# Optimization experiments

Measured on AMD Instinct MI355X. Metric: run time of the kernel, lower is better.

The kernel has to match this reference:

```python
import jax, jax.numpy as jnp
import numpy as np

N_CLASSES = 80
SEG_LEN = 512          # boxes per class (uniform segments)
H = 128                # hidden_size
DH = 2 * H             # decoder hidden (= concat of bidirectional encoder final hiddens)
EMB = 32               # decoder_input_dim
SOS, EOS = 2, 3


def _gru_cell(x, h, Wih, Whh, bih, bhh):
    # PyTorch GRU cell math. x:(in,), h:(hid,), Wih:(3*hid,in), Whh:(3*hid,hid)
    gi = Wih @ x + bih
    gh = Whh @ h + bhh
    i_r, i_z, i_n = jnp.split(gi, 3)
    h_r, h_z, h_n = jnp.split(gh, 3)
    r = jax.nn.sigmoid(i_r + h_r)
    z = jax.nn.sigmoid(i_z + h_z)
    n = jnp.tanh(i_n + r * h_n)
    return (1.0 - z) * n + z * h


def _gru_seq(xs, h0, Wih, Whh, bih, bhh):
    # xs: (T, in); returns final hidden (hid,) and all hiddens (T, hid)
    def step(h, x):
        h2 = _gru_cell(x, h, Wih, Whh, bih, bhh)
        return h2, h2
    hT, hs = jax.lax.scan(step, h0, xs)
    return hT, hs

# vmap over the 80 classes (per-class weights)
_run_gru = jax.vmap(_gru_seq, in_axes=(0, 0, 0, 0, 0, 0))


def setup_inputs() -> dict:
    key = jax.random.key(0)
    ks = jax.random.split(key, 32)
    N = N_CLASSES * SEG_LEN
    s = 0.05
    inp = {
        "feat": jax.random.normal(ks[0], (N, 1024), jnp.float32),
        "score": jax.random.uniform(ks[1], (N, 1), jnp.float32),
        "box": jax.random.uniform(ks[2], (N, 4), jnp.float32),
        "origin_score": jax.random.uniform(ks[3], (N, 91), jnp.float32),
        "labels": jax.random.randint(ks[4], (N,), 0, 2, jnp.int64),
        "weights": jax.random.uniform(ks[5], (N,), jnp.float32),
        "unique_class": jnp.ones((N_CLASSES,), jnp.int64),
        "unique_class_len": jnp.arange(N_CLASSES + 1, dtype=jnp.int64) * SEG_LEN,
        # shared linears
        "appear_W": jax.random.normal(ks[6], (H, 1024), jnp.float32) * s,
        "appear_b": jnp.zeros((H,), jnp.float32),
        "featlin_W": jax.random.normal(ks[7], (H, H + 96), jnp.float32) * s,
        "featlin_b": jnp.zeros((H,), jnp.float32),
        # per-class bidirectional encoder GRUs
        "enc_Wih_f": jax.random.normal(ks[8], (N_CLASSES, 3 * H, H), jnp.float32) * s,
        "enc_Whh_f": jax.random.normal(ks[9], (N_CLASSES, 3 * H, H), jnp.float32) * s,
        "enc_bih_f": jnp.zeros((N_CLASSES, 3 * H), jnp.float32),
        "enc_bhh_f": jnp.zeros((N_CLASSES, 3 * H), jnp.float32),
        "enc_Wih_b": jax.random.normal(ks[10], (N_CLASSES, 3 * H, H), jnp.float32) * s,
        "enc_Whh_b": jax.random.normal(ks[11], (N_CLASSES, 3 * H, H), jnp.float32) * s,
        "enc_bih_b": jnp.zeros((N_CLASSES, 3 * H), jnp.float32),
        "enc_bhh_b": jnp.zeros((N_CLASSES, 3 * H), jnp.float32),
        # decoder
        "dec_emb": jax.random.normal(ks[12], (4, EMB), jnp.float32) * s,
        "dec_Wih": jax.random.normal(ks[13], (N_CLASSES, 3 * DH, EMB), jnp.float32) * s,
        "dec_Whh": jax.random.normal(ks[14], (N_CLASSES, 3 * DH, DH), jnp.float32) * s,
        "dec_bih": jnp.zeros((N_CLASSES, 3 * DH), jnp.float32),
        "dec_bhh": jnp.zeros((N_CLASSES, 3 * DH), jnp.float32),
        "out_W": jax.random.normal(ks[15], (4, DH), jnp.float32) * s,
        "out_b": jnp.zeros((4,), jnp.float32),
    }
    return inp


def reference(feat, score, box, origin_score, labels, weights, unique_class,
              unique_class_len, appear_W, appear_b, featlin_W, featlin_b,
              enc_Wih_f, enc_Whh_f, enc_bih_f, enc_bhh_f,
              enc_Wih_b, enc_Whh_b, enc_bih_b, enc_bhh_b,
              dec_emb, dec_Wih, dec_Whh, dec_bih, dec_bhh, out_W, out_b):
    # --- shared feature encoding ---
    x = jax.nn.relu(feat @ appear_W.T + appear_b)                    # (N, H)
    allf = jnp.concatenate([x, score, box, origin_score], axis=1)    # (N, H+96)
    enc_feat = jax.nn.relu(allf @ featlin_W.T + featlin_b)           # (N, H)

    # --- per-class bidirectional encoder (uniform segments) ---
    seg = enc_feat.reshape(N_CLASSES, SEG_LEN, H)
    eos = jnp.ones((N_CLASSES, 1, H), enc_feat.dtype)                # encoder_EOS = ones
    enc_in = jnp.concatenate([seg, eos], axis=1)                     # (80, L+1, H)
    h0 = jnp.zeros((N_CLASSES, H), enc_feat.dtype)
    h_f, _ = _run_gru(enc_in, h0, enc_Wih_f, enc_Whh_f, enc_bih_f, enc_bhh_f)
    h_b, _ = _run_gru(enc_in[:, ::-1], h0, enc_Wih_b, enc_Whh_b, enc_bih_b, enc_bhh_b)
    dec_h0 = jnp.concatenate([h_f, h_b], axis=-1)                    # (80, 2H)

    # --- per-class decoder with teacher forcing (SOS then gold labels) ---
    emb = dec_emb[labels].reshape(N_CLASSES, SEG_LEN, EMB)
    sos = jnp.broadcast_to(dec_emb[SOS], (N_CLASSES, 1, EMB))
    dec_in = jnp.concatenate([sos, emb], axis=1)                     # (80, L+1, EMB)
    _, dec_hs = _run_gru(dec_in, dec_h0, dec_Wih, dec_Whh, dec_bih, dec_bhh)

    logits = dec_hs.reshape(-1, DH) @ out_W.T + out_b                # (80*(L+1), 4)
    output = jax.nn.log_softmax(logits, axis=-1)
    return output, labels, weights
```

## Files before the change

kernel.cpp:

```cpp
#include <hip/hip_runtime.h>


typedef __fp16 h2v __attribute__((ext_vector_type(2)));
typedef __fp16 h8 __attribute__((ext_vector_type(8)));

__device__ __forceinline__ h2v pk2(float a, float b) {
  return __builtin_amdgcn_cvt_pkrtz(a, b);
}
__device__ __forceinline__ unsigned h2u(h2v h) { return __builtin_bit_cast(unsigned, h); }
__device__ __forceinline__ h2v u2h(unsigned u) { return __builtin_bit_cast(h2v, u); }
__device__ __forceinline__ float fdot2f(h2v a, h2v b, float c) {
  return __builtin_amdgcn_fdot2(a, b, c, false);
}
__device__ __forceinline__ float sigf(float x) { return 1.f / (1.f + __expf(-x)); }
__device__ __forceinline__ float tanhfast(float x) { return 2.f / (1.f + __expf(-2.f * x)) - 1.f; }

__device__ __forceinline__ h8 pack8(float4 a, float4 b) {
  h2v p0 = pk2(a.x, a.y), p1 = pk2(a.z, a.w), p2 = pk2(b.x, b.y), p3 = pk2(b.z, b.w);
  return (h8){p0[0], p0[1], p1[0], p1[1], p2[0], p2[1], p3[0], p3[1]};
}

#define SL(V, j) (__builtin_shufflevector((V), (V), 2 * (j), 2 * (j) + 1))

template <int CTRL>
__device__ __forceinline__ float dppadd(float acc, float v) {
  int r = __builtin_amdgcn_update_dpp(0, __float_as_int(v), CTRL, 0xF, 0xF, true);
  return acc + __int_as_float(r);
}
__device__ __forceinline__ float swz4add(float acc, float v) {
  return acc + __int_as_float(__builtin_amdgcn_ds_swizzle(__float_as_int(v), 0x101F));
}

__device__ __forceinline__ float reduce8s(float p0, float p1, float p2, float p3,
                                          float p4, float p5, float p6, float p7) {
  p0 = dppadd<0xB1>(p0, p1);
  p2 = dppadd<0xB1>(p2, p3);
  p4 = dppadd<0xB1>(p4, p5);
  p6 = dppadd<0xB1>(p6, p7);
  p0 = dppadd<0x4E>(p0, p2);
  p4 = dppadd<0x4E>(p4, p6);
  p0 = swz4add(p0, p4);
  p0 = dppadd<0x128>(p0, p0);
  return p0;
}

__device__ __forceinline__ float dot4(h8 V, h2v a0, h2v a1, h2v a2, h2v a3, float acc) {
  acc = fdot2f(SL(V, 0), a0, acc);
  acc = fdot2f(SL(V, 1), a1, acc);
  acc = fdot2f(SL(V, 2), a2, acc);
  acc = fdot2f(SL(V, 3), a3, acc);
  return acc;
}

__global__ void k_fill_misc(const float* __restrict__ score, const float* __restrict__ box,
                            const float* __restrict__ orig, float* __restrict__ allf) {
  int i = blockIdx.x * blockDim.x + threadIdx.x;
  if (i >= 40960 * 96) return;
  int row = i / 96, k = i - row * 96;
  float v;
  if (k == 0) v = score[row];
  else if (k < 5) v = box[row * 4 + (k - 1)];
  else v = orig[(size_t)row * 91 + (k - 5)];
  allf[(size_t)row * 224 + 128 + k] = v;
}

__global__ __launch_bounds__(256) void k_gemm_appear(
    const float* __restrict__ A, const float* __restrict__ W,
    const float* __restrict__ bias, float* __restrict__ allf) {
  __shared__ float As[32][68];
  __shared__ float Ws[32][132];
  const int tid = threadIdx.x;
  const int tx = tid & 15, ty = tid >> 4;
  const int r0 = blockIdx.x * 64;
  const int lr = tid >> 3;
  const int lk = (tid & 7) * 4;
  float acc[4][8];
#pragma unroll
  for (int i = 0; i < 4; ++i)
#pragma unroll
    for (int j = 0; j < 8; ++j) acc[i][j] = 0.f;

  for (int k0 = 0; k0 < 1024; k0 += 32) {
#pragma unroll
    for (int i = 0; i < 2; ++i) {
      int rr = lr + i * 32;
      float4 v = *(const float4*)(A + (size_t)(r0 + rr) * 1024 + k0 + lk);
      As[lk + 0][rr] = v.x; As[lk + 1][rr] = v.y; As[lk + 2][rr] = v.z; As[lk + 3][rr] = v.w;
    }
#pragma unroll
    for (int i = 0; i < 4; ++i) {
      int wr = lr + i * 32;
      float4 v = *(const float4*)(W + (size_t)wr * 1024 + k0 + lk);
      Ws[lk + 0][wr] = v.x; Ws[lk + 1][wr] = v.y; Ws[lk + 2][wr] = v.z; Ws[lk + 3][wr] = v.w;
    }
    __syncthreads();
#pragma unroll
    for (int kk = 0; kk < 32; ++kk) {
      float4 a = *(const float4*)&As[kk][ty * 4];
      float4 w0 = *(const float4*)&Ws[kk][tx * 8];
      float4 w1 = *(const float4*)&Ws[kk][tx * 8 + 4];
      float av[4] = {a.x, a.y, a.z, a.w};
      float wv[8] = {w0.x, w0.y, w0.z, w0.w, w1.x, w1.y, w1.z, w1.w};
#pragma unroll
      for (int i = 0; i < 4; ++i)
#pragma unroll
        for (int j = 0; j < 8; ++j) acc[i][j] = fmaf(av[i], wv[j], acc[i][j]);
    }
    __syncthreads();
  }
#pragma unroll
  for (int i = 0; i < 4; ++i) {
    int row = r0 + ty * 4 + i;
#pragma unroll
    for (int j = 0; j < 8; ++j) {
      int col = tx * 8 + j;
      float v = acc[i][j] + bias[col];
      allf[(size_t)row * 224 + col] = fmaxf(v, 0.f);
    }
  }
}

__global__ __launch_bounds__(256) void k_gemm_featlin(
    const float* __restrict__ A, const float* __restrict__ W,
    const float* __restrict__ bias, unsigned* __restrict__ encf2) {
  __shared__ float As[32][68];
  __shared__ float Ws[32][132];
  const int tid = threadIdx.x;
  const int tx = tid & 15, ty = tid >> 4;
  const int r0 = blockIdx.x * 64;
  const int lr = tid >> 3;
  const int lk = (tid & 7) * 4;
  float acc[4][8];
#pragma unroll
  for (int i = 0; i < 4; ++i)
#pragma unroll
    for (int j = 0; j < 8; ++j) acc[i][j] = 0.f;

  for (int k0 = 0; k0 < 224; k0 += 32) {
#pragma unroll
    for (int i = 0; i < 2; ++i) {
      int rr = lr + i * 32;
      float4 v = *(const float4*)(A + (size_t)(r0 + rr) * 224 + k0 + lk);
      As[lk + 0][rr] = v.x; As[lk + 1][rr] = v.y; As[lk + 2][rr] = v.z; As[lk + 3][rr] = v.w;
    }
#pragma unroll
    for (int i = 0; i < 4; ++i) {
      int wr = lr + i * 32;
      float4 v = *(const float4*)(W + (size_t)wr * 224 + k0 + lk);
      Ws[lk + 0][wr] = v.x; Ws[lk + 1][wr] = v.y; Ws[lk + 2][wr] = v.z; Ws[lk + 3][wr] = v.w;
    }
    __syncthreads();
#pragma unroll
    for (int kk = 0; kk < 32; ++kk) {
      float4 a = *(const float4*)&As[kk][ty * 4];
      float4 w0 = *(const float4*)&Ws[kk][tx * 8];
      float4 w1 = *(const float4*)&Ws[kk][tx * 8 + 4];
      float av[4] = {a.x, a.y, a.z, a.w};
      float wv[8] = {w0.x, w0.y, w0.z, w0.w, w1.x, w1.y, w1.z, w1.w};
#pragma unroll
      for (int i = 0; i < 4; ++i)
#pragma unroll
        for (int j = 0; j < 8; ++j) acc[i][j] = fmaf(av[i], wv[j], acc[i][j]);
    }
    __syncthreads();
  }
#pragma unroll
  for (int i = 0; i < 4; ++i) {
    int row = r0 + ty * 4 + i;
    unsigned* orow = encf2 + (size_t)row * 64;
#pragma unroll
    for (int p = 0; p < 4; ++p) {
      int col = tx * 8 + 2 * p;
      float a = fmaxf(acc[i][2 * p] + bias[col], 0.f);
      float b = fmaxf(acc[i][2 * p + 1] + bias[col + 1], 0.f);
      orow[tx * 4 + p] = h2u(pk2(a, b));
    }
  }
}

__global__ __launch_bounds__(256) void k_dec_gi(
    const float* __restrict__ Wih, const float* __restrict__ bih,
    const float* __restrict__ emb, float* __restrict__ gi) {
  __shared__ float e[4][32];
  const int c = blockIdx.x, tid = threadIdx.x;
  if (tid < 128) e[tid >> 5][tid & 31] = emb[tid];
  __syncthreads();
#pragma unroll
  for (int i = 0; i < 3; ++i) {
    int r = tid + i * 256;
    const float* w = Wih + ((size_t)c * 768 + r) * 32;
    float b = bih[(size_t)c * 768 + r];
    float a0 = b, a1 = b, a2 = b, a3 = b;
#pragma unroll
    for (int k = 0; k < 32; ++k) {
      float wv = w[k];
      a0 = fmaf(wv, e[0][k], a0);
      a1 = fmaf(wv, e[1][k], a1);
      a2 = fmaf(wv, e[2][k], a2);
      a3 = fmaf(wv, e[3][k], a3);
    }
    gi[((size_t)c * 4 + 0) * 768 + r] = a0;
    gi[((size_t)c * 4 + 1) * 768 + r] = a1;
    gi[((size_t)c * 4 + 2) * 768 + r] = a2;
    gi[((size_t)c * 4 + 3) * 768 + r] = a3;
  }
}

__global__ __launch_bounds__(768) void k_pack_dec(
    const float* __restrict__ Whh, uint4* __restrict__ wpk) {
  const int c = blockIdx.x >> 5, ic = blockIdx.x & 31;
  const int tid = threadIdx.x;
  const int w = tid >> 6, l = tid & 63, q = l >> 4, m = l & 15, mw = m & 7;
  const int kc = ic >> 4, kk = (ic >> 1) & 7, half = ic & 1;
  const int row = 64 * w + 16 * q + 8 * kc + (kk ^ mw);
  const float* src = Whh + ((size_t)c * 768 + row) * 256 + 16 * m + 8 * half;
  float4 a = *(const float4*)(src);
  float4 b = *(const float4*)(src + 4);
  uint4 o;
  o.x = h2u(pk2(a.x, a.y));
  o.y = h2u(pk2(a.z, a.w));
  o.z = h2u(pk2(b.x, b.y));
  o.w = h2u(pk2(b.z, b.w));
  wpk[((size_t)c * 32 + ic) * 768 + tid] = o;
}

#define ENCROW(k)                                                                   \
  h8 ci_##k, ch_##k, sg_##k;                                                        \
  {                                                                                 \
    int vc = 32 * w + 8 * q + ((k) ^ mw);                                           \
    const float4* pi = (const float4*)(Wih + (size_t)vc * 128 + 8 * m);             \
    ci_##k = pack8(pi[0], pi[1]);                                                   \
    __builtin_amdgcn_sched_barrier(0);                                              \
    const float4* ph = (const float4*)(Whh + (size_t)vc * 128 + 8 * m);             \
    ch_##k = pack8(ph[0], ph[1]);                                                   \
    __builtin_amdgcn_sched_barrier(0);                                              \
    int s = (w < 4) ? vc : (vc - 128);                                              \
    const float* sb =                                                               \
        (w < 4) ? (Wih + (size_t)(256 + s) * 128) : (Whh + (size_t)(256 + s) * 128);\
    const float4* ps = (const float4*)(sb + 8 * m);                                 \
    sg_##k = pack8(ps[0], ps[1]);                                                   \
    __builtin_amdgcn_sched_barrier(0);                                              \
  }

#define EDOTC(k) dot4(ci_##k, x0, x1, x2, x3, dot4(ch_##k, g0, g1, g2, g3, 0.f))
#define EDOTS(k) dot4(sg_##k, s0, s1, s2, s3, 0.f)

__global__ __launch_bounds__(512) void k_enc_gru(
    const unsigned* __restrict__ encf2,
    const float* __restrict__ WihF, const float* __restrict__ WhhF,
    const float* __restrict__ bihF, const float* __restrict__ bhhF,
    const float* __restrict__ WihB, const float* __restrict__ WhhB,
    const float* __restrict__ bihB, const float* __restrict__ bhhB,
    float* __restrict__ dec_h0) {
  const int blk = blockIdx.x;
  const int c = blk >> 1, dir = blk & 1;
  const int tid = threadIdx.x;
  const int w = tid >> 6, l = tid & 63, q = l >> 4, m = l & 15, mw = m & 7;

  const float* Wih = (dir ? WihB : WihF) + (size_t)c * 384 * 128;
  const float* Whh = (dir ? WhhB : WhhF) + (size_t)c * 384 * 128;
  const float* bih = (dir ? bihB : bihF) + (size_t)c * 384;
  const float* bhh = (dir ? bhhB : bhhF) + (size_t)c * 384;

  __shared__ __align__(16) unsigned x2s[2][64];
  __shared__ __align__(16) unsigned h2s[64];
  __shared__ float aBuf[512];

  ENCROW(0) ENCROW(1) ENCROW(2) ENCROW(3)
  ENCROW(4) ENCROW(5) ENCROW(6) ENCROW(7)

  float bown;
  int ownIdx;
  if (m < 8) {
    int vo = 32 * w + 8 * q + m;
    bown = bih[vo] + bhh[vo];
    ownIdx = vo;
  } else {
    int so = (w < 4) ? (32 * w + 8 * q + mw) : (32 * (w - 4) + 8 * q + mw);
    bown = (w < 4) ? bih[256 + so] : bhh[256 + so];
    ownIdx = (w < 4) ? (256 + so) : (384 + so);
  }

  if (tid < 64) h2s[tid] = 0u;
  if (tid >= 448) {
    int lane = tid - 448;
    x2s[0][lane] = (dir == 0) ? encf2[((size_t)c * 512 + 0) * 64 + lane] : 0x3C003C00u;
  }
  float hreg = 0.f;
  __syncthreads();

  for (int t = 0; t <= 512; ++t) {
    unsigned xpre = 0;
    if (tid >= 448 && t < 512) {
      int tn = t + 1, lane = tid - 448;
      int row = (dir == 0) ? ((tn < 512) ? tn : -1) : (512 - tn);
      xpre = (row < 0) ? 0x3C003C00u : encf2[((size_t)c * 512 + row) * 64 + lane];
    }
    uint4 xv = ((const uint4*)&x2s[t & 1][0])[m];
    uint4 hv = ((const uint4*)&h2s[0])[m];
    h2v x0 = u2h(xv.x), x1 = u2h(xv.y), x2 = u2h(xv.z), x3 = u2h(xv.w);
    h2v g0 = u2h(hv.x), g1 = u2h(hv.y), g2 = u2h(hv.z), g3 = u2h(hv.w);
    float pA = reduce8s(EDOTC(0), EDOTC(1), EDOTC(2), EDOTC(3),
                        EDOTC(4), EDOTC(5), EDOTC(6), EDOTC(7));
    h2v s0 = (w < 4) ? x0 : g0, s1 = (w < 4) ? x1 : g1;
    h2v s2 = (w < 4) ? x2 : g2, s3 = (w < 4) ? x3 : g3;
    float pB = reduce8s(EDOTS(0), EDOTS(1), EDOTS(2), EDOTS(3),
                        EDOTS(4), EDOTS(5), EDOTS(6), EDOTS(7));
    aBuf[ownIdx] = ((m < 8) ? pA : pB) + bown;
    __syncthreads();
    if (tid < 128) {
      float r = sigf(aBuf[tid]);
      float z = sigf(aBuf[128 + tid]);
      float nn = tanhfast(aBuf[256 + tid] + r * aBuf[384 + tid]);
      float hn = (1.f - z) * nn + z * hreg;
      hreg = hn;
      float other = __shfl_xor(hn, 1, 64);
      if ((tid & 1) == 0) h2s[tid >> 1] = h2u(pk2(hn, other));
    } else if (tid >= 448 && t < 512) {
      x2s[(t + 1) & 1][tid - 448] = xpre;
    }
    __syncthreads();
  }
  if (tid < 128) dec_h0[(size_t)c * 256 + dir * 128 + tid] = hreg;
}

#define CONS(sa, sb, dst)                                   \
  {                                                         \
    float a_ = 0.f;                                         \
    a_ = fdot2f(u2h((sa).x), g0, a_);                       \
    a_ = fdot2f(u2h((sa).y), g1, a_);                       \
    a_ = fdot2f(u2h((sa).z), g2, a_);                       \
    a_ = fdot2f(u2h((sa).w), g3, a_);                       \
    a_ = fdot2f(u2h((sb).x), g4, a_);                       \
    a_ = fdot2f(u2h((sb).y), g5, a_);                       \
    a_ = fdot2f(u2h((sb).z), g6, a_);                       \
    a_ = fdot2f(u2h((sb).w), g7, a_);                       \
    dst = a_;                                               \
  }

#define DITER(P, J, D)                                      \
  CONS(bA##P, bB##P, D);                                    \
  bA##P = wp[((2 * (J) + 8) & 31) * 768];                   \
  bB##P = wp[((2 * (J) + 9) & 31) * 768];

#define BAR_LGKM()                                          \
  asm volatile("s_waitcnt lgkmcnt(0)" ::: "memory");        \
  __builtin_amdgcn_s_barrier();                             \
  asm volatile("" ::: "memory");

__global__ __launch_bounds__(768) void k_dec_gru(
    const uint4* __restrict__ wpk, const float* __restrict__ bhh,
    const float* __restrict__ gi, const float* __restrict__ h0,
    const int* __restrict__ labels,
    const float* __restrict__ outW, const float* __restrict__ outB,
    float* __restrict__ out) {
  const int c = blockIdx.x, tid = threadIdx.x;
  const int w = tid >> 6, l = tid & 63, m = l & 15;

  __shared__ __align__(16) unsigned h2s[128];
  __shared__ float aBuf[768];
  __shared__ float gisf[2304];
  __shared__ float owsh[1024];
  __shared__ int labs[513];
  __shared__ float red[4][4];

  const uint4* wp = wpk + (size_t)c * 32 * 768 + tid;
  uint4 bA0 = wp[0 * 768], bB0 = wp[1 * 768];
  uint4 bA1 = wp[2 * 768], bB1 = wp[3 * 768];
  uint4 bA2 = wp[4 * 768], bB2 = wp[5 * 768];
  uint4 bA3 = wp[6 * 768], bB3 = wp[7 * 768];

  float bown = bhh[(size_t)c * 768 + 64 * w + l];
  for (int i = tid; i < 2304; i += 768) gisf[i] = gi[(size_t)c * 4 * 768 + i];
  for (int i = tid; i < 1024; i += 768) owsh[i] = outW[i];
  if (tid < 512) labs[tid + 1] = labels[(size_t)c * 512 + tid];
  if (tid == 512) labs[0] = 2;
  float b0 = outB[0], b1 = outB[1], b2 = outB[2], b3 = outB[3];
  float hreg = 0.f;
  if (tid < 256) {
    hreg = h0[(size_t)c * 256 + tid];
    float other = __shfl_xor(hreg, 1, 64);
    if ((tid & 1) == 0) h2s[tid >> 1] = h2u(pk2(hreg, other));
  }
  __syncthreads();

  for (int t = 0; t <= 512; ++t) {
    const uint4* hp = (const uint4*)(&h2s[0]);
    uint4 ha = hp[2 * m], hb = hp[2 * m + 1];
    h2v g0 = u2h(ha.x), g1 = u2h(ha.y), g2 = u2h(ha.z), g3 = u2h(ha.w);
    h2v g4 = u2h(hb.x), g5 = u2h(hb.y), g6 = u2h(hb.z), g7 = u2h(hb.w);
    float s0, s1, s2, s3, s4, s5, s6, s7;
    DITER(0, 0, s0) DITER(1, 1, s1) DITER(2, 2, s2) DITER(3, 3, s3)
    DITER(0, 4, s4) DITER(1, 5, s5) DITER(2, 6, s6) DITER(3, 7, s7)
    float pc0 = reduce8s(s0, s1, s2, s3, s4, s5, s6, s7);
    DITER(0, 8, s0) DITER(1, 9, s1) DITER(2, 10, s2) DITER(3, 11, s3)
    DITER(0, 12, s4) DITER(1, 13, s5) DITER(2, 14, s6) DITER(3, 15, s7)
    float pc1 = reduce8s(s0, s1, s2, s3, s4, s5, s6, s7);
    aBuf[64 * w + l] = ((m < 8) ? pc0 : pc1) + bown;
    BAR_LGKM();
    if (tid < 256) {
      int sel = labs[t];
      const float* gsel = &gisf[sel * 768];
      float r = sigf(gsel[tid] + aBuf[tid]);
      float z = sigf(gsel[256 + tid] + aBuf[256 + tid]);
      float nn = tanhfast(gsel[512 + tid] + r * aBuf[512 + tid]);
      float hn = (1.f - z) * nn + z * hreg;
      hreg = hn;
      float other = __shfl_xor(hn, 1, 64);
      if ((tid & 1) == 0) h2s[tid >> 1] = h2u(pk2(hn, other));
      float p0 = owsh[tid] * hn, p1 = owsh[256 + tid] * hn;
      float p2 = owsh[512 + tid] * hn, p3 = owsh[768 + tid] * hn;
#pragma unroll
      for (int off = 32; off > 0; off >>= 1) {
        p0 += __shfl_xor(p0, off, 64);
        p1 += __shfl_xor(p1, off, 64);
        p2 += __shfl_xor(p2, off, 64);
        p3 += __shfl_xor(p3, off, 64);
      }
      if ((tid & 63) == 0) {
        int ww = tid >> 6;
        red[ww][0] = p0; red[ww][1] = p1; red[ww][2] = p2; red[ww][3] = p3;
      }
    }
    BAR_LGKM();
    if (tid == 0) {
      float l0 = red[0][0] + red[1][0] + red[2][0] + red[3][0] + b0;
      float l1 = red[0][1] + red[1][1] + red[2][1] + red[3][1] + b1;
      float l2 = red[0][2] + red[1][2] + red[2][2] + red[3][2] + b2;
      float l3 = red[0][3] + red[1][3] + red[2][3] + red[3][3] + b3;
      float mm = fmaxf(fmaxf(l0, l1), fmaxf(l2, l3));
      float s = __expf(l0 - mm) + __expf(l1 - mm) + __expf(l2 - mm) + __expf(l3 - mm);
      float lse = mm + __logf(s);
      float* o = out + ((size_t)c * 513 + t) * 4;
      o[0] = l0 - lse; o[1] = l1 - lse; o[2] = l2 - lse; o[3] = l3 - lse;
    }
  }
}

__global__ void k_passthrough(const int* __restrict__ labels,
                              const float* __restrict__ weights,
                              float* __restrict__ out) {
  int i = blockIdx.x * blockDim.x + threadIdx.x;
  if (i < 40960) {
    out[164160 + i] = (float)labels[i];
    out[164160 + 40960 + i] = weights[i];
  }
}

extern "C" void kernel_launch(void* const* d_in, const int* in_sizes, int n_in,
                              void* d_out, int out_size, void* d_ws, size_t ws_size,
                              hipStream_t stream) {
  (void)in_sizes; (void)n_in; (void)out_size; (void)ws_size;
  const float* feat = (const float*)d_in[0];
  const float* score = (const float*)d_in[1];
  const float* box = (const float*)d_in[2];
  const float* orig = (const float*)d_in[3];
  const int* labels = (const int*)d_in[4];
  const float* weights = (const float*)d_in[5];
  const float* appear_W = (const float*)d_in[8];
  const float* appear_b = (const float*)d_in[9];
  const float* featlin_W = (const float*)d_in[10];
  const float* featlin_b = (const float*)d_in[11];
  const float* eWihF = (const float*)d_in[12];
  const float* eWhhF = (const float*)d_in[13];
  const float* ebihF = (const float*)d_in[14];
  const float* ebhhF = (const float*)d_in[15];
  const float* eWihB = (const float*)d_in[16];
  const float* eWhhB = (const float*)d_in[17];
  const float* ebihB = (const float*)d_in[18];
  const float* ebhhB = (const float*)d_in[19];
  const float* dec_emb = (const float*)d_in[20];
  const float* dWih = (const float*)d_in[21];
  const float* dWhh = (const float*)d_in[22];
  const float* dbih = (const float*)d_in[23];
  const float* dbhh = (const float*)d_in[24];
  const float* outW = (const float*)d_in[25];
  const float* outB = (const float*)d_in[26];
  float* out = (float*)d_out;

  char* ws = (char*)d_ws;
  float* allf = (float*)ws;
  unsigned* encf2 = (unsigned*)(ws + (size_t)40960 * 224 * 4);
  float* dec_h0 = (float*)(ws + (size_t)40960 * 224 * 4 + (size_t)40960 * 64 * 4);
  float* dec_gi = dec_h0 + 80 * 256;
  uint4* wpack = (uint4*)allf;

  k_fill_misc<<<15360, 256, 0, stream>>>(score, box, orig, allf);
  k_gemm_appear<<<640, 256, 0, stream>>>(feat, appear_W, appear_b, allf);
  k_gemm_featlin<<<640, 256, 0, stream>>>(allf, featlin_W, featlin_b, encf2);
  k_pack_dec<<<80 * 32, 768, 0, stream>>>(dWhh, wpack);
  k_dec_gi<<<80, 256, 0, stream>>>(dWih, dbih, dec_emb, dec_gi);
  k_enc_gru<<<160, 512, 0, stream>>>(encf2, eWihF, eWhhF, ebihF, ebhhF,
                                     eWihB, eWhhB, ebihB, ebhhB, dec_h0);
  k_dec_gru<<<80, 768, 0, stream>>>(wpack, dbhh, dec_gi, dec_h0, labels, outW, outB, out);
  k_passthrough<<<160, 256, 0, stream>>>(labels, weights, out);
}
```

Before: 1.819 ms.

## Split recurrent GRU weights across registers, LDS and streamed global loads

```diff
diff --git a/kernel.cpp b/kernel.cpp
--- a/kernel.cpp
+++ b/kernel.cpp
@@ -2,7 +2,6 @@
 
 
 typedef __fp16 h2v __attribute__((ext_vector_type(2)));
-typedef __fp16 h8 __attribute__((ext_vector_type(8)));
 
 __device__ __forceinline__ h2v pk2(float a, float b) {
   return __builtin_amdgcn_cvt_pkrtz(a, b);
@@ -15,12 +14,21 @@
 __device__ __forceinline__ float sigf(float x) { return 1.f / (1.f + __expf(-x)); }
 __device__ __forceinline__ float tanhfast(float x) { return 2.f / (1.f + __expf(-2.f * x)) - 1.f; }
 
-__device__ __forceinline__ h8 pack8(float4 a, float4 b) {
-  h2v p0 = pk2(a.x, a.y), p1 = pk2(a.z, a.w), p2 = pk2(b.x, b.y), p3 = pk2(b.z, b.w);
-  return (h8){p0[0], p0[1], p1[0], p1[1], p2[0], p2[1], p3[0], p3[1]};
-}
-
-#define SL(V, j) (__builtin_shufflevector((V), (V), 2 * (j), 2 * (j) + 1))
+__device__ __forceinline__ uint4 pack8u(float4 a, float4 b) {
+  uint4 o;
+  o.x = h2u(pk2(a.x, a.y)); o.y = h2u(pk2(a.z, a.w));
+  o.z = h2u(pk2(b.x, b.y)); o.w = h2u(pk2(b.z, b.w));
+  return o;
+}
+
+__device__ __forceinline__ float dotu4(uint4 cv, h2v a0, h2v a1, h2v a2, h2v a3,
+                                       float acc) {
+  acc = fdot2f(u2h(cv.x), a0, acc);
+  acc = fdot2f(u2h(cv.y), a1, acc);
+  acc = fdot2f(u2h(cv.z), a2, acc);
+  acc = fdot2f(u2h(cv.w), a3, acc);
+  return acc;
+}
 
 template <int CTRL>
 __device__ __forceinline__ float dppadd(float acc, float v) {
@@ -29,27 +37,6 @@
 }
 __device__ __forceinline__ float swz4add(float acc, float v) {
   return acc + __int_as_float(__builtin_amdgcn_ds_swizzle(__float_as_int(v), 0x101F));
-}
-
-__device__ __forceinline__ float reduce8s(float p0, float p1, float p2, float p3,
-                                          float p4, float p5, float p6, float p7) {
-  p0 = dppadd<0xB1>(p0, p1);
-  p2 = dppadd<0xB1>(p2, p3);
-  p4 = dppadd<0xB1>(p4, p5);
-  p6 = dppadd<0xB1>(p6, p7);
-  p0 = dppadd<0x4E>(p0, p2);
-  p4 = dppadd<0x4E>(p4, p6);
-  p0 = swz4add(p0, p4);
-  p0 = dppadd<0x128>(p0, p0);
-  return p0;
-}
-
-__device__ __forceinline__ float dot4(h8 V, h2v a0, h2v a1, h2v a2, h2v a3, float acc) {
-  acc = fdot2f(SL(V, 0), a0, acc);
-  acc = fdot2f(SL(V, 1), a1, acc);
-  acc = fdot2f(SL(V, 2), a2, acc);
-  acc = fdot2f(SL(V, 3), a3, acc);
-  return acc;
 }
 
 __global__ void k_fill_misc(const float* __restrict__ score, const float* __restrict__ box,
@@ -216,34 +203,47 @@
   const float* src = Whh + ((size_t)c * 768 + row) * 256 + 16 * m + 8 * half;
   float4 a = *(const float4*)(src);
   float4 b = *(const float4*)(src + 4);
-  uint4 o;
-  o.x = h2u(pk2(a.x, a.y));
-  o.y = h2u(pk2(a.z, a.w));
-  o.z = h2u(pk2(b.x, b.y));
-  o.w = h2u(pk2(b.z, b.w));
-  wpk[((size_t)c * 32 + ic) * 768 + tid] = o;
-}
-
-#define ENCROW(k)                                                                   \
-  h8 ci_##k, ch_##k, sg_##k;                                                        \
-  {                                                                                 \
-    int vc = 32 * w + 8 * q + ((k) ^ mw);                                           \
-    const float4* pi = (const float4*)(Wih + (size_t)vc * 128 + 8 * m);             \
-    ci_##k = pack8(pi[0], pi[1]);                                                   \
-    __builtin_amdgcn_sched_barrier(0);                                              \
-    const float4* ph = (const float4*)(Whh + (size_t)vc * 128 + 8 * m);             \
-    ch_##k = pack8(ph[0], ph[1]);                                                   \
-    __builtin_amdgcn_sched_barrier(0);                                              \
-    int s = (w < 4) ? vc : (vc - 128);                                              \
-    const float* sb =                                                               \
-        (w < 4) ? (Wih + (size_t)(256 + s) * 128) : (Whh + (size_t)(256 + s) * 128);\
-    const float4* ps = (const float4*)(sb + 8 * m);                                 \
-    sg_##k = pack8(ps[0], ps[1]);                                                   \
-    __builtin_amdgcn_sched_barrier(0);                                              \
-  }
-
-#define EDOTC(k) dot4(ci_##k, x0, x1, x2, x3, dot4(ch_##k, g0, g1, g2, g3, 0.f))
-#define EDOTS(k) dot4(sg_##k, s0, s1, s2, s3, 0.f)
+  wpk[((size_t)c * 32 + ic) * 768 + tid] = pack8u(a, b);
+}
+
+#define LD_CI(k)                                                              \
+  uint4 ci_##k;                                                               \
+  { int vc = 32 * w + 8 * q + ((k) ^ mw);                                     \
+    const float4* pi = (const float4*)(Wih + (size_t)vc * 128 + 8 * m);       \
+    ci_##k = pack8u(pi[0], pi[1]); }                                          \
+  __builtin_amdgcn_sched_barrier(0);
+
+#define LD_CH_REG(k)                                                          \
+  uint4 ch_##k;                                                               \
+  { int vc = 32 * w + 8 * q + ((k) ^ mw);                                     \
+    const float4* ph = (const float4*)(Whh + (size_t)vc * 128 + 8 * m);       \
+    ch_##k = pack8u(ph[0], ph[1]); }                                          \
+  __builtin_amdgcn_sched_barrier(0);
+
+#define LD_CH_LDS(k)                                                          \
+  { int vc = 32 * w + 8 * q + ((k) ^ mw);                                     \
+    const float4* ph = (const float4*)(Whh + (size_t)vc * 128 + 8 * m);       \
+    wle[((k) - 1) * 512 + tid] = pack8u(ph[0], ph[1]); }                      \
+  __builtin_amdgcn_sched_barrier(0);
+
+#define LD_SG_REG(k)                                                          \
+  uint4 sg_##k;                                                               \
+  { int vc = 32 * w + 8 * q + ((k) ^ mw);                                     \
+    int s = (w < 4) ? vc : (vc - 128);                                        \
+    const float* sb2 = (w < 4) ? (Wih + (size_t)(256 + s) * 128)              \
+                               : (Whh + (size_t)(256 + s) * 128);             \
+    const float4* ps = (const float4*)(sb2 + 8 * m);                          \
+    sg_##k = pack8u(ps[0], ps[1]); }                                          \
+  __builtin_amdgcn_sched_barrier(0);
+
+#define LD_SG_LDS(k)                                                          \
+  { int vc = 32 * w + 8 * q + ((k) ^ mw);                                     \
+    int s = (w < 4) ? vc : (vc - 128);                                        \
+    const float* sb2 = (w < 4) ? (Wih + (size_t)(256 + s) * 128)              \
+                               : (Whh + (size_t)(256 + s) * 128);             \
+    const float4* ps = (const float4*)(sb2 + 8 * m);                          \
+    wle[(7 + (k) - 4) * 512 + tid] = pack8u(ps[0], ps[1]); }                  \
+  __builtin_amdgcn_sched_barrier(0);
 
 __global__ __launch_bounds__(512) void k_enc_gru(
     const unsigned* __restrict__ encf2,
@@ -265,9 +265,14 @@
   __shared__ __align__(16) unsigned x2s[2][64];
   __shared__ __align__(16) unsigned h2s[64];
   __shared__ float aBuf[512];
-
-  ENCROW(0) ENCROW(1) ENCROW(2) ENCROW(3)
-  ENCROW(4) ENCROW(5) ENCROW(6) ENCROW(7)
+  __shared__ uint4 wle[11 * 512];
+
+  LD_CI(0) LD_CI(1) LD_CI(2) LD_CI(3) LD_CI(4) LD_CI(5) LD_CI(6) LD_CI(7)
+  LD_CH_REG(0)
+  LD_CH_LDS(1) LD_CH_LDS(2) LD_CH_LDS(3) LD_CH_LDS(4)
+  LD_CH_LDS(5) LD_CH_LDS(6) LD_CH_LDS(7)
+  LD_SG_REG(0) LD_SG_REG(1) LD_SG_REG(2) LD_SG_REG(3)
+  LD_SG_LDS(4) LD_SG_LDS(5) LD_SG_LDS(6) LD_SG_LDS(7)
 
   float bown;
   int ownIdx;
@@ -289,6 +294,8 @@
   float hreg = 0.f;
   __syncthreads();
 
+  const uint4* wl = wle + tid;
+
   for (int t = 0; t <= 512; ++t) {
     unsigned xpre = 0;
     if (tid >= 448 && t < 512) {
@@ -300,12 +307,52 @@
     uint4 hv = ((const uint4*)&h2s[0])[m];
     h2v x0 = u2h(xv.x), x1 = u2h(xv.y), x2 = u2h(xv.z), x3 = u2h(xv.w);
     h2v g0 = u2h(hv.x), g1 = u2h(hv.y), g2 = u2h(hv.z), g3 = u2h(hv.w);
-    float pA = reduce8s(EDOTC(0), EDOTC(1), EDOTC(2), EDOTC(3),
-                        EDOTC(4), EDOTC(5), EDOTC(6), EDOTC(7));
+    float p0 = dotu4(ci_0, x0, x1, x2, x3, dotu4(ch_0, g0, g1, g2, g3, 0.f));
+    uint4 cv = wl[0 * 512];
+    float p1 = dotu4(ci_1, x0, x1, x2, x3, dotu4(cv, g0, g1, g2, g3, 0.f));
+    p0 = dppadd<0xB1>(p0, p1);
+    cv = wl[1 * 512];
+    float p2 = dotu4(ci_2, x0, x1, x2, x3, dotu4(cv, g0, g1, g2, g3, 0.f));
+    cv = wl[2 * 512];
+    float p3 = dotu4(ci_3, x0, x1, x2, x3, dotu4(cv, g0, g1, g2, g3, 0.f));
+    p2 = dppadd<0xB1>(p2, p3);
+    p0 = dppadd<0x4E>(p0, p2);
+    cv = wl[3 * 512];
+    float p4 = dotu4(ci_4, x0, x1, x2, x3, dotu4(cv, g0, g1, g2, g3, 0.f));
+    cv = wl[4 * 512];
+    float p5 = dotu4(ci_5, x0, x1, x2, x3, dotu4(cv, g0, g1, g2, g3, 0.f));
+    p4 = dppadd<0xB1>(p4, p5);
+    cv = wl[5 * 512];
+    float p6 = dotu4(ci_6, x0, x1, x2, x3, dotu4(cv, g0, g1, g2, g3, 0.f));
+    cv = wl[6 * 512];
+    float p7 = dotu4(ci_7, x0, x1, x2, x3, dotu4(cv, g0, g1, g2, g3, 0.f));
+    p6 = dppadd<0xB1>(p6, p7);
+    p4 = dppadd<0x4E>(p4, p6);
+    p0 = swz4add(p0, p4);
+    float pA = dppadd<0x128>(p0, p0);
     h2v s0 = (w < 4) ? x0 : g0, s1 = (w < 4) ? x1 : g1;
     h2v s2 = (w < 4) ? x2 : g2, s3 = (w < 4) ? x3 : g3;
-    float pB = reduce8s(EDOTS(0), EDOTS(1), EDOTS(2), EDOTS(3),
-                        EDOTS(4), EDOTS(5), EDOTS(6), EDOTS(7));
+    float q0 = dotu4(sg_0, s0, s1, s2, s3, 0.f);
+    float q1 = dotu4(sg_1, s0, s1, s2, s3, 0.f);
+    q0 = dppadd<0xB1>(q0, q1);
+    float q2 = dotu4(sg_2, s0, s1, s2, s3, 0.f);
+    float q3 = dotu4(sg_3, s0, s1, s2, s3, 0.f);
+    q2 = dppadd<0xB1>(q2, q3);
+    q0 = dppadd<0x4E>(q0, q2);
+    cv = wl[7 * 512];
+    float q4 = dotu4(cv, s0, s1, s2, s3, 0.f);
+    cv = wl[8 * 512];
+    float q5 = dotu4(cv, s0, s1, s2, s3, 0.f);
+    q4 = dppadd<0xB1>(q4, q5);
+    cv = wl[9 * 512];
+    float q6 = dotu4(cv, s0, s1, s2, s3, 0.f);
+    cv = wl[10 * 512];
+    float q7 = dotu4(cv, s0, s1, s2, s3, 0.f);
+    q6 = dppadd<0xB1>(q6, q7);
+    q4 = dppadd<0x4E>(q4, q6);
+    q0 = swz4add(q0, q4);
+    float pB = dppadd<0x128>(q0, q0);
+
     aBuf[ownIdx] = ((m < 8) ? pA : pB) + bown;
     __syncthreads();
     if (tid < 128) {
@@ -324,28 +371,12 @@
   if (tid < 128) dec_h0[(size_t)c * 256 + dir * 128 + tid] = hreg;
 }
 
-#define CONS(sa, sb, dst)                                   \
-  {                                                         \
-    float a_ = 0.f;                                         \
-    a_ = fdot2f(u2h((sa).x), g0, a_);                       \
-    a_ = fdot2f(u2h((sa).y), g1, a_);                       \
-    a_ = fdot2f(u2h((sa).z), g2, a_);                       \
-    a_ = fdot2f(u2h((sa).w), g3, a_);                       \
-    a_ = fdot2f(u2h((sb).x), g4, a_);                       \
-    a_ = fdot2f(u2h((sb).y), g5, a_);                       \
-    a_ = fdot2f(u2h((sb).z), g6, a_);                       \
-    a_ = fdot2f(u2h((sb).w), g7, a_);                       \
-    dst = a_;                                               \
-  }
-
-#define DITER(P, J, D)                                      \
-  CONS(bA##P, bB##P, D);                                    \
-  bA##P = wp[((2 * (J) + 8) & 31) * 768];                   \
-  bB##P = wp[((2 * (J) + 9) & 31) * 768];
-
-#define BAR_LGKM()                                          \
-  asm volatile("s_waitcnt lgkmcnt(0)" ::: "memory");        \
-  __builtin_amdgcn_s_barrier();                             \
+#define CONSX(sa, sb, dst)                                                    \
+  dst = dotu4(sb, g4, g5, g6, g7, dotu4(sa, g0, g1, g2, g3, 0.f));
+
+#define BAR_LGKM()                                                            \
+  asm volatile("s_waitcnt lgkmcnt(0)" ::: "memory");                          \
+  __builtin_amdgcn_s_barrier();                                               \
   asm volatile("" ::: "memory");
 
 __global__ __launch_bounds__(768) void k_dec_gru(
@@ -359,19 +390,25 @@
 
   __shared__ __align__(16) unsigned h2s[128];
   __shared__ float aBuf[768];
-  __shared__ float gisf[2304];
   __shared__ float owsh[1024];
   __shared__ int labs[513];
   __shared__ float red[4][4];
+  __shared__ uint4 wlds[12 * 768];
 
   const uint4* wp = wpk + (size_t)c * 32 * 768 + tid;
-  uint4 bA0 = wp[0 * 768], bB0 = wp[1 * 768];
-  uint4 bA1 = wp[2 * 768], bB1 = wp[3 * 768];
-  uint4 bA2 = wp[4 * 768], bB2 = wp[5 * 768];
-  uint4 bA3 = wp[6 * 768], bB3 = wp[7 * 768];
+  const uint4* wps = wp + 24 * 768;
+
+  for (int j = 0; j < 12; ++j) wlds[j * 768 + tid] = wp[(12 + j) * 768];
+  __builtin_amdgcn_sched_barrier(0);
+  uint4 ua0 = wp[0 * 768], ua1 = wp[1 * 768], ua2 = wp[2 * 768], ua3 = wp[3 * 768];
+  uint4 ua4 = wp[4 * 768], ua5 = wp[5 * 768], ua6 = wp[6 * 768], ua7 = wp[7 * 768];
+  uint4 ua8 = wp[8 * 768], ua9 = wp[9 * 768], ua10 = wp[10 * 768], ua11 = wp[11 * 768];
+  __builtin_amdgcn_sched_barrier(0);
+  uint4 sl0 = wps[0 * 768], sl1 = wps[1 * 768];
+  uint4 sl2 = wps[2 * 768], sl3 = wps[3 * 768];
 
   float bown = bhh[(size_t)c * 768 + 64 * w + l];
-  for (int i = tid; i < 2304; i += 768) gisf[i] = gi[(size_t)c * 4 * 768 + i];
+  const float* gib = gi + (size_t)c * 4 * 768;
   for (int i = tid; i < 1024; i += 768) owsh[i] = outW[i];
   if (tid < 512) labs[tid + 1] = labels[(size_t)c * 512 + tid];
   if (tid == 512) labs[0] = 2;
@@ -384,42 +421,70 @@
   }
   __syncthreads();
 
+  const uint4* wl = wlds + tid;
+
   for (int t = 0; t <= 512; ++t) {
-    const uint4* hp = (const uint4*)(&h2s[0]);
-    uint4 ha = hp[2 * m], hb = hp[2 * m + 1];
+    uint4 ha = ((const uint4*)h2s)[2 * m];
+    uint4 hb = ((const uint4*)h2s)[2 * m + 1];
     h2v g0 = u2h(ha.x), g1 = u2h(ha.y), g2 = u2h(ha.z), g3 = u2h(ha.w);
     h2v g4 = u2h(hb.x), g5 = u2h(hb.y), g6 = u2h(hb.z), g7 = u2h(hb.w);
-    float s0, s1, s2, s3, s4, s5, s6, s7;
-    DITER(0, 0, s0) DITER(1, 1, s1) DITER(2, 2, s2) DITER(3, 3, s3)
-    DITER(0, 4, s4) DITER(1, 5, s5) DITER(2, 6, s6) DITER(3, 7, s7)
-    float pc0 = reduce8s(s0, s1, s2, s3, s4, s5, s6, s7);
-    DITER(0, 8, s0) DITER(1, 9, s1) DITER(2, 10, s2) DITER(3, 11, s3)
-    DITER(0, 12, s4) DITER(1, 13, s5) DITER(2, 14, s6) DITER(3, 15, s7)
-    float pc1 = reduce8s(s0, s1, s2, s3, s4, s5, s6, s7);
+    float p4s, p5s, p6s, p7s;
+    CONSX(sl0, sl1, p4s); sl0 = wps[4 * 768]; sl1 = wps[5 * 768];
+    CONSX(sl2, sl3, p5s); sl2 = wps[6 * 768]; sl3 = wps[7 * 768];
+    float q4 = dppadd<0xB1>(p4s, p5s);
+    __builtin_amdgcn_sched_barrier(0);
+    int sel = labs[t];
+    float gv0 = 0.f, gv1 = 0.f, gv2 = 0.f;
+    if (tid < 256) {
+      const float* gp = gib + sel * 768;
+      gv0 = gp[tid]; gv1 = gp[tid + 256]; gv2 = gp[tid + 512];
+    }
+    float p0, p1, p2, p3;
+    CONSX(ua0, ua1, p0); CONSX(ua2, ua3, p1); p0 = dppadd<0xB1>(p0, p1);
+    CONSX(ua4, ua5, p2); CONSX(ua6, ua7, p3); p2 = dppadd<0xB1>(p2, p3);
+    p0 = dppadd<0x4E>(p0, p2);
+    CONSX(ua8, ua9, p2); CONSX(ua10, ua11, p3); p2 = dppadd<0xB1>(p2, p3);
+    uint4 cw0 = wl[0 * 768], cw1 = wl[1 * 768], cw2 = wl[2 * 768], cw3 = wl[3 * 768];
+    float p6b, p7b;
+    CONSX(cw0, cw1, p6b); CONSX(cw2, cw3, p7b); p6b = dppadd<0xB1>(p6b, p7b);
+    p2 = dppadd<0x4E>(p2, p6b);
+    p0 = swz4add(p0, p2);
+    float pc0 = dppadd<0x128>(p0, p0);
+    CONSX(sl0, sl1, p6s); sl0 = wps[0 * 768]; sl1 = wps[1 * 768];
+    __builtin_amdgcn_sched_barrier(0);
+    cw0 = wl[4 * 768]; cw1 = wl[5 * 768]; cw2 = wl[6 * 768]; cw3 = wl[7 * 768];
+    CONSX(cw0, cw1, p0); CONSX(cw2, cw3, p1); p0 = dppadd<0xB1>(p0, p1);
+    cw0 = wl[8 * 768]; cw1 = wl[9 * 768]; cw2 = wl[10 * 768]; cw3 = wl[11 * 768];
+    CONSX(cw0, cw1, p2); CONSX(cw2, cw3, p3); p2 = dppadd<0xB1>(p2, p3);
+    p0 = dppadd<0x4E>(p0, p2);
+    CONSX(sl2, sl3, p7s); sl2 = wps[2 * 768]; sl3 = wps[3 * 768];
+    float q6 = dppadd<0xB1>(p6s, p7s);
+    q4 = dppadd<0x4E>(q4, q6);
+    p0 = swz4add(p0, q4);
+    float pc1 = dppadd<0x128>(p0, p0);
+
     aBuf[64 * w + l] = ((m < 8) ? pc0 : pc1) + bown;
     BAR_LGKM();
     if (tid < 256) {
-      int sel = labs[t];
-      const float* gsel = &gisf[sel * 768];
-      float r = sigf(gsel[tid] + aBuf[tid]);
-      float z = sigf(gsel[256 + tid] + aBuf[256 + tid]);
-      float nn = tanhfast(gsel[512 + tid] + r * aBuf[512 + tid]);
+      float r = sigf(gv0 + aBuf[tid]);
+      float z = sigf(gv1 + aBuf[256 + tid]);
+      float nn = tanhfast(gv2 + r * aBuf[512 + tid]);
       float hn = (1.f - z) * nn + z * hreg;
       hreg = hn;
       float other = __shfl_xor(hn, 1, 64);
       if ((tid & 1) == 0) h2s[tid >> 1] = h2u(pk2(hn, other));
-      float p0 = owsh[tid] * hn, p1 = owsh[256 + tid] * hn;
-      float p2 = owsh[512 + tid] * hn, p3 = owsh[768 + tid] * hn;
+      float p0o = owsh[tid] * hn, p1o = owsh[256 + tid] * hn;
+      float p2o = owsh[512 + tid] * hn, p3o = owsh[768 + tid] * hn;
 #pragma unroll
       for (int off = 32; off > 0; off >>= 1) {
-        p0 += __shfl_xor(p0, off, 64);
-        p1 += __shfl_xor(p1, off, 64);
-        p2 += __shfl_xor(p2, off, 64);
-        p3 += __shfl_xor(p3, off, 64);
+        p0o += __shfl_xor(p0o, off, 64);
+        p1o += __shfl_xor(p1o, off, 64);
+        p2o += __shfl_xor(p2o, off, 64);
+        p3o += __shfl_xor(p3o, off, 64);
       }
       if ((tid & 63) == 0) {
         int ww = tid >> 6;
-        red[ww][0] = p0; red[ww][1] = p1; red[ww][2] = p2; red[ww][3] = p3;
+        red[ww][0] = p0o; red[ww][1] = p1o; red[ww][2] = p2o; red[ww][3] = p3o;
       }
     }
     BAR_LGKM();
```

After: 1.697 ms. 1.07x faster.
